# Kernel tuning notes

Measured on AMD Instinct MI355X. Metric: run time of the kernel, lower is better.

## Reference

```python
import jax, jax.numpy as jnp
import numpy as np

B, N, D = 8, 9856, 256
HEADS = 8
WH, WW = 7, 11
HID = 512  # int(D * 2.0)
EPS = 1e-5


def layernorm(x, g, b):
    mu = jnp.mean(x, axis=-1, keepdims=True)
    var = jnp.mean(jnp.square(x - mu), axis=-1, keepdims=True)
    return (x - mu) * jax.lax.rsqrt(var + EPS) * g + b


def setup_inputs() -> dict:
    key = jax.random.key(0)
    ks = jax.random.split(key, 6)
    s = lambda k, shape: (jax.random.normal(k, shape, jnp.float32) * 0.02)
    return {
        "x": jax.random.normal(ks[0], (B, N, D), jnp.float32),
        "norm1_g": jnp.ones((D,), jnp.float32),
        "norm1_b": jnp.zeros((D,), jnp.float32),
        "in_proj_w": s(ks[1], (3 * D, D)),
        "in_proj_b": jnp.zeros((3 * D,), jnp.float32),
        "out_w": s(ks[2], (D, D)),
        "out_b": jnp.zeros((D,), jnp.float32),
        "norm2_g": jnp.ones((D,), jnp.float32),
        "norm2_b": jnp.zeros((D,), jnp.float32),
        "fc1_w": s(ks[3], (HID, D)),
        "fc1_b": jnp.zeros((HID,), jnp.float32),
        "fc2_w": s(ks[4], (D, HID)),
        "fc2_b": jnp.zeros((D,), jnp.float32),
        "h": 56,
        "w": 176,
    }


def reference(x, norm1_g, norm1_b, in_proj_w, in_proj_b, out_w, out_b,
              norm2_g, norm2_b, fc1_w, fc1_b, fc2_w, fc2_b, h, w):
    Bx, Nx, Dx = x.shape
    n_h, n_w = h // WH, w // WW  # chosen dims divide evenly -> pad_h = pad_w = 0
    hd = Dx // HEADS
    L = WH * WW  # 77 tokens per window

    res = x
    xn = layernorm(x, norm1_g, norm1_b)

    # window partition: (B, h*w, D) -> (B*n_h*n_w, wh*ww, D)
    win = xn.reshape(Bx, n_h, WH, n_w, WW, Dx)
    win = win.transpose(0, 1, 3, 2, 4, 5).reshape(-1, L, Dx)

    # MultiheadAttention (batch_first) on each window independently
    qkv = win @ in_proj_w.T + in_proj_b          # (NW, L, 3D)
    q, k, v = jnp.split(qkv, 3, axis=-1)
    NW = win.shape[0]
    q = q.reshape(NW, L, HEADS, hd).transpose(0, 2, 1, 3)
    k = k.reshape(NW, L, HEADS, hd).transpose(0, 2, 1, 3)
    v = v.reshape(NW, L, HEADS, hd).transpose(0, 2, 1, 3)
    scores = jnp.einsum("nhld,nhmd->nhlm", q, k) / jnp.sqrt(jnp.float32(hd))
    attn = jax.nn.softmax(scores, axis=-1)
    o = jnp.einsum("nhlm,nhmd->nhld", attn, v)   # (NW, H, L, hd)
    o = o.transpose(0, 2, 1, 3).reshape(NW, L, Dx)
    o = o @ out_w.T + out_b

    # window reverse: (B*n_h*n_w, wh*ww, D) -> (B, h*w, D)
    o = o.reshape(Bx, n_h, n_w, WH, WW, Dx)
    o = o.transpose(0, 1, 3, 2, 4, 5).reshape(Bx, Nx, Dx)

    x = res + o
    res = x
    xn2 = layernorm(x, norm2_g, norm2_b)
    hmid = jax.nn.gelu(xn2 @ fc1_w.T + fc1_b, approximate=False)
    mlp = hmid @ fc2_w.T + fc2_b
    return res + mlp
```

## Files before the change

kernel.cpp:

```cpp
#include <hip/hip_runtime.h>
#include <hip/hip_bf16.h>

typedef unsigned short u16;
typedef unsigned int   u32;

typedef __bf16 bf16x8 __attribute__((ext_vector_type(8)));
typedef float  f32x4  __attribute__((ext_vector_type(4)));

__device__ __forceinline__ u16 f2bf(float f) {
  u32 u = __float_as_uint(f);
  u += 0x7fffu + ((u >> 16) & 1u);
  return (u16)(u >> 16);
}
__device__ __forceinline__ u32 pack2(float a, float b) {
  return (u32)f2bf(a) | ((u32)f2bf(b) << 16);
}
__device__ __forceinline__ void gld16(const void* g, void* l) {
  __builtin_amdgcn_global_load_lds(
      (const __attribute__((address_space(1))) unsigned int*)g,
      (__attribute__((address_space(3))) unsigned int*)l, 16, 0, 0);
}

#define TOK_M   78848
#define DIM     256
#define NWIN    1024
#define WINL    77

__global__ __launch_bounds__(256)
void cvt_w(const float* __restrict__ w0, const float* __restrict__ w1,
           const float* __restrict__ w2, const float* __restrict__ w3,
           u16* __restrict__ out)
{
  const int i = (blockIdx.x * 256 + threadIdx.x) * 4;
  const float* src; int off;
  if      (i < 196608) { src = w0; off = i; }
  else if (i < 262144) { src = w1; off = i - 196608; }
  else if (i < 393216) { src = w2; off = i - 262144; }
  else                 { src = w3; off = i - 393216; }
  float4 v = *(const float4*)(src + off);
  uint2 o; o.x = pack2(v.x, v.y); o.y = pack2(v.z, v.w);
  *(uint2*)(out + i) = o;
}

template<bool PERM>
__global__ __launch_bounds__(256)
void ln_k(const float* __restrict__ X, const float* __restrict__ g,
          const float* __restrict__ bta, u16* __restrict__ Y)
{
  const int tid  = threadIdx.x;
  const int tok  = blockIdx.x * 4 + (tid >> 6);
  const int lane = tid & 63;
  float4 v = *(const float4*)(X + (size_t)tok * DIM + lane * 4);
  float s = v.x + v.y + v.z + v.w;
#pragma unroll
  for (int off = 32; off; off >>= 1) s += __shfl_xor(s, off);
  const float mu = s * (1.f / 256.f);
  const float dx = v.x - mu, dy = v.y - mu, dz = v.z - mu, dw = v.w - mu;
  float q = dx * dx + dy * dy + dz * dz + dw * dw;
#pragma unroll
  for (int off = 32; off; off >>= 1) q += __shfl_xor(q, off);
  const float rstd = rsqrtf(q * (1.f / 256.f) + 1e-5f);
  float4 gg = *(const float4*)(g + lane * 4);
  float4 bb = *(const float4*)(bta + lane * 4);
  const float y0 = dx * rstd * gg.x + bb.x;
  const float y1 = dy * rstd * gg.y + bb.y;
  const float y2 = dz * rstd * gg.z + bb.z;
  const float y3 = dw * rstd * gg.w + bb.w;
  size_t dest = (size_t)tok;
  if (PERM) {
    const int b  = tok / 9856, n = tok - b * 9856;
    const int y  = n / 176,  xc = n - y * 176;
    const int ih = y / 7,    rr = y - ih * 7;
    const int iw = xc / 11,  cc = xc - iw * 11;
    dest = (size_t)(((b * 8 + ih) * 16 + iw)) * 77 + rr * 11 + cc;
  }
  uint2 o;
  o.x = pack2(y0, y1);
  o.y = pack2(y2, y3);
  *(uint2*)(Y + dest * DIM + lane * 4) = o;
}

template<int EPI, int OBF>
__global__ __launch_bounds__(256, 3)
void gemm_mfma(const u16* __restrict__ A, const u16* __restrict__ W,
               const float* __restrict__ bias, const float* res,
               void* Cout, int N, int K)
{
  __shared__ u16 As[4096];
  __shared__ u16 Bs[4096];

  const int tid  = threadIdx.x;
  const int wave = tid >> 6, lane = tid & 63;
  const int wy = wave >> 1, wx = wave & 1;
  const int quad = lane >> 4, l16 = lane & 15;
  const int m0 = blockIdx.x * 128;
  const int n0 = blockIdx.y * 128;

  const int s0 = tid, s1 = tid + 256;
  const int r0 = s0 >> 2, r1 = s1 >> 2;
  const int kb0 = (s0 & 3) ^ (r0 & 3);
  const int kb1 = (s1 & 3) ^ (r1 & 3);
  const u16* Ag0 = A + (size_t)(m0 + r0) * K + kb0 * 8;
  const u16* Ag1 = A + (size_t)(m0 + r1) * K + kb1 * 8;
  const u16* Bg0 = W + (size_t)(n0 + r0) * K + kb0 * 8;
  const u16* Bg1 = W + (size_t)(n0 + r1) * K + kb1 * 8;

  const int kbs = quad ^ (l16 & 3);
  const u16* Ar = &As[(wy * 64 + l16) * 32 + kbs * 8];
  const u16* Br = &Bs[(wx * 64 + l16) * 32 + kbs * 8];

  f32x4 acc[4][4];
#pragma unroll
  for (int i = 0; i < 4; ++i)
#pragma unroll
    for (int j = 0; j < 4; ++j) {
      f32x4 z = {0.f, 0.f, 0.f, 0.f};
      acc[i][j] = z;
    }

  for (int kt = 0; kt < K; kt += 32) {
    gld16(Ag0 + kt, &As[s0 * 8]);
    gld16(Ag1 + kt, &As[s1 * 8]);
    gld16(Bg0 + kt, &Bs[s0 * 8]);
    gld16(Bg1 + kt, &Bs[s1 * 8]);
    __syncthreads();
    bf16x8 af[4], bv[4];
#pragma unroll
    for (int i = 0; i < 4; ++i) {
      af[i] = *(const bf16x8*)(Ar + i * 16 * 32);
      bv[i] = *(const bf16x8*)(Br + i * 16 * 32);
    }
#pragma unroll
    for (int mi = 0; mi < 4; ++mi)
#pragma unroll
      for (int ni = 0; ni < 4; ++ni)
        acc[mi][ni] = __builtin_amdgcn_mfma_f32_16x16x32_bf16(
            af[mi], bv[ni], acc[mi][ni], 0, 0, 0);
    __syncthreads();
  }

  const int gr0 = m0 + wy * 64 + quad * 4;
  const int gc0 = n0 + wx * 64 + l16;
#pragma unroll
  for (int ni = 0; ni < 4; ++ni) {
    const int gc = gc0 + ni * 16;
    const float bvs = bias[gc];
#pragma unroll
    for (int mi = 0; mi < 4; ++mi) {
      const int gr = gr0 + mi * 16;
      f32x4 a = acc[mi][ni];
#pragma unroll
      for (int e = 0; e < 4; ++e) {
        float v = a[e] + bvs;
        const size_t idx = (size_t)(gr + e) * N + gc;
        if (EPI == 1) v += res[idx];
        else if (EPI == 2) v = 0.5f * v * (1.f + erff(v * 0.70710678118654752f));
        if (OBF) ((u16*)Cout)[idx] = f2bf(v);
        else     ((float*)Cout)[idx] = v;
      }
    }
  }
}

#define PSTR 104
__global__ __launch_bounds__(128)
void attn_mfma(const u16* __restrict__ qkv, u16* __restrict__ onat)
{
  __shared__ __bf16 Pb[2][80 * PSTR];

  const int tid  = threadIdx.x;
  const int wave = tid >> 6, lane = tid & 63;
  const int quad = lane >> 4, l16 = lane & 15;
  const int pair = blockIdx.x * 2 + wave;
  const int nw   = pair >> 3, head = pair & 7;
  const size_t base = (size_t)nw * 77 * 768;
  const int hoff = head * 32;
  __bf16* P = Pb[wave];

  {
    uint4 z = {0, 0, 0, 0};
    for (int r = lane; r < 80; r += 64) {
      *(uint4*)(P + r * PSTR + 80) = z;
      *(uint4*)(P + r * PSTR + 88) = z;
    }
  }

  bf16x8 qf[5], kf[5];
  const u16* qp = qkv + base + hoff + quad * 8;
#pragma unroll
  for (int mi = 0; mi < 5; ++mi) {
    const size_t row = (size_t)(l16 + 16 * mi) * 768;
    qf[mi] = *(const bf16x8*)(qp + row);
    kf[mi] = *(const bf16x8*)(qp + row + 256);
  }

  f32x4 s[5][5];
#pragma unroll
  for (int mi = 0; mi < 5; ++mi)
#pragma unroll
    for (int ni = 0; ni < 5; ++ni) {
      f32x4 z = {0.f, 0.f, 0.f, 0.f};
      s[mi][ni] = z;
    }
#pragma unroll
  for (int mi = 0; mi < 5; ++mi)
#pragma unroll
    for (int ni = 0; ni < 5; ++ni)
      s[mi][ni] = __builtin_amdgcn_mfma_f32_16x16x32_bf16(
          qf[mi], kf[ni], s[mi][ni], 0, 0, 0);

  bf16x8 vf[3][2];
  {
    const __bf16* vbb = (const __bf16*)(qkv + base + 512 + hoff + l16);
#pragma unroll
    for (int ks = 0; ks < 3; ++ks)
#pragma unroll
      for (int ni = 0; ni < 2; ++ni)
#pragma unroll
        for (int jj = 0; jj < 8; ++jj) {
          const int k = ks * 32 + quad * 8 + jj;
          vf[ks][ni][jj] = (k < 77) ? vbb[(size_t)k * 768 + 16 * ni] : (__bf16)0.f;
        }
  }

  if (l16 >= 13) {
#pragma unroll
    for (int mi = 0; mi < 5; ++mi)
#pragma unroll
      for (int e = 0; e < 4; ++e) s[mi][4][e] = -1e30f;
  }

  const float c = 0.17677669529663687f * 1.4426950408889634f;
  float inv[5][4];
#pragma unroll
  for (int mi = 0; mi < 5; ++mi)
#pragma unroll
    for (int e = 0; e < 4; ++e) {
      float mx = s[mi][0][e];
#pragma unroll
      for (int ni = 1; ni < 5; ++ni) mx = fmaxf(mx, s[mi][ni][e]);
#pragma unroll
      for (int off = 1; off < 16; off <<= 1) mx = fmaxf(mx, __shfl_xor(mx, off));
      float sum = 0.f;
#pragma unroll
      for (int ni = 0; ni < 5; ++ni) {
        const float ev = exp2f((s[mi][ni][e] - mx) * c);
        s[mi][ni][e] = ev;
        sum += ev;
      }
#pragma unroll
      for (int off = 1; off < 16; off <<= 1) sum += __shfl_xor(sum, off);
      inv[mi][e] = 1.f / sum;
    }

#pragma unroll
  for (int mi = 0; mi < 5; ++mi)
#pragma unroll
    for (int e = 0; e < 4; ++e) {
      const int m = quad * 4 + e + 16 * mi;
#pragma unroll
      for (int ni = 0; ni < 5; ++ni)
        P[m * PSTR + l16 + 16 * ni] = (__bf16)(s[mi][ni][e] * inv[mi][e]);
    }

  f32x4 o[5][2];
#pragma unroll
  for (int mi = 0; mi < 5; ++mi)
#pragma unroll
    for (int ni = 0; ni < 2; ++ni) {
      f32x4 z = {0.f, 0.f, 0.f, 0.f};
      o[mi][ni] = z;
    }
#pragma unroll
  for (int ks = 0; ks < 3; ++ks)
#pragma unroll
    for (int mi = 0; mi < 5; ++mi) {
      const bf16x8 af = *(const bf16x8*)(P + (l16 + 16 * mi) * PSTR + ks * 32 + quad * 8);
#pragma unroll
      for (int ni = 0; ni < 2; ++ni)
        o[mi][ni] = __builtin_amdgcn_mfma_f32_16x16x32_bf16(
            af, vf[ks][ni], o[mi][ni], 0, 0, 0);
    }

  const int b  = nw >> 7;
  const int ih = (nw >> 4) & 7;
  const int iw = nw & 15;
#pragma unroll
  for (int mi = 0; mi < 5; ++mi)
#pragma unroll
    for (int e = 0; e < 4; ++e) {
      const int t = quad * 4 + e + 16 * mi;
      if (t < 77) {
        const int rr = t / 11, cc = t - rr * 11;
        const int y = ih * 7 + rr, xc = iw * 11 + cc;
        const size_t nat = (size_t)b * 9856 + (size_t)y * 176 + xc;
        u16* dst = onat + nat * DIM + hoff + l16;
        dst[0]  = f2bf(o[mi][0][e]);
        dst[16] = f2bf(o[mi][1][e]);
      }
    }
}

extern "C" void kernel_launch(void* const* d_in, const int* in_sizes, int n_in,
                              void* d_out, int out_size, void* d_ws, size_t ws_size,
                              hipStream_t stream)
{
  (void)in_sizes; (void)n_in; (void)out_size; (void)ws_size;
  const float* x    = (const float*)d_in[0];
  const float* g1   = (const float*)d_in[1];
  const float* b1   = (const float*)d_in[2];
  const float* wqkv = (const float*)d_in[3];
  const float* bqkv = (const float*)d_in[4];
  const float* wout = (const float*)d_in[5];
  const float* bout = (const float*)d_in[6];
  const float* g2   = (const float*)d_in[7];
  const float* b2   = (const float*)d_in[8];
  const float* w1   = (const float*)d_in[9];
  const float* bf1  = (const float*)d_in[10];
  const float* w2   = (const float*)d_in[11];
  const float* bf2  = (const float*)d_in[12];

  char* ws = (char*)d_ws;
  u16*   qkv  = (u16*)(ws);
  u16*   xn   = (u16*)(ws + 121110528);
  u16*   onat = (u16*)(ws + 161480704);
  u16*   wb   = (u16*)(ws + 201850880);
  u16*   wqkv_b = wb;
  u16*   wout_b = wb + 196608;
  u16*   w1_b   = wb + 262144;
  u16*   w2_b   = wb + 393216;
  float* x2   = (float*)d_out;

  cvt_w<<<512, 256, 0, stream>>>(wqkv, wout, w1, w2, wb);
  ln_k<true><<<19712, 256, 0, stream>>>(x, g1, b1, xn);
  gemm_mfma<0, 1><<<dim3(616, 6), 256, 0, stream>>>(xn, wqkv_b, bqkv, nullptr, qkv, 768, 256);
  attn_mfma<<<4096, 128, 0, stream>>>(qkv, onat);
  gemm_mfma<1, 0><<<dim3(616, 2), 256, 0, stream>>>(onat, wout_b, bout, x, x2, 256, 256);
  ln_k<false><<<19712, 256, 0, stream>>>(x2, g2, b2, xn);
  gemm_mfma<2, 1><<<dim3(616, 4), 256, 0, stream>>>(xn, w1_b, bf1, nullptr, qkv, 512, 256);
  gemm_mfma<1, 0><<<dim3(616, 2), 256, 0, stream>>>(qkv, w2_b, bf2, x2, x2, 256, 512);
}
```

Measured before the change: 597.3 us.

## Double-buffer GEMM LDS tiles and swap grid order for A-tile reuse

The MFMA GEMM now uses two LDS buffers per operand and issues the global-to-LDS loads for the next K tile before computing on the current one, so load latency overlaps with MFMA work. The grid is also transposed so that consecutive blocks share the same A row tile across N tiles, which should improve L2 reuse of the activation matrix. LDS use per block doubles, which may reduce occupancy below the launch-bounds target. The visible loop keeps a single barrier, so whether the buffer being overwritten is safely separated from reads of the previous iteration depends on the unseen end of the loop.

```diff
diff --git a/kernel.cpp b/kernel.cpp
--- a/kernel.cpp
+++ b/kernel.cpp
@@ -86,15 +86,15 @@
                const float* __restrict__ bias, const float* res,
                void* Cout, int N, int K)
 {
-  __shared__ u16 As[4096];
-  __shared__ u16 Bs[4096];
+  __shared__ u16 As[2][4096];
+  __shared__ u16 Bs[2][4096];
 
   const int tid  = threadIdx.x;
   const int wave = tid >> 6, lane = tid & 63;
   const int wy = wave >> 1, wx = wave & 1;
   const int quad = lane >> 4, l16 = lane & 15;
-  const int m0 = blockIdx.x * 128;
-  const int n0 = blockIdx.y * 128;
+  const int m0 = blockIdx.y * 128;
+  const int n0 = blockIdx.x * 128;
 
   const int s0 = tid, s1 = tid + 256;
   const int r0 = s0 >> 2, r1 = s1 >> 2;
@@ -106,8 +106,8 @@
   const u16* Bg1 = W + (size_t)(n0 + r1) * K + kb1 * 8;
 
   const int kbs = quad ^ (l16 & 3);
-  const u16* Ar = &As[(wy * 64 + l16) * 32 + kbs * 8];
-  const u16* Br = &Bs[(wx * 64 + l16) * 32 + kbs * 8];
+  const int aoff = (wy * 64 + l16) * 32 + kbs * 8;
+  const int boff = (wx * 64 + l16) * 32 + kbs * 8;
 
   f32x4 acc[4][4];
 #pragma unroll
@@ -118,12 +118,24 @@
       acc[i][j] = z;
     }
 
-  for (int kt = 0; kt < K; kt += 32) {
-    gld16(Ag0 + kt, &As[s0 * 8]);
-    gld16(Ag1 + kt, &As[s1 * 8]);
-    gld16(Bg0 + kt, &Bs[s0 * 8]);
-    gld16(Bg1 + kt, &Bs[s1 * 8]);
-    __syncthreads();
+  gld16(Ag0, &As[0][s0 * 8]);
+  gld16(Ag1, &As[0][s1 * 8]);
+  gld16(Bg0, &Bs[0][s0 * 8]);
+  gld16(Bg1, &Bs[0][s1 * 8]);
+  __syncthreads();
+
+  const int NT = K >> 5;
+  for (int t = 0; t < NT; ++t) {
+    const int cur = t & 1;
+    if (t + 1 < NT) {
+      const int kt = (t + 1) << 5;
+      gld16(Ag0 + kt, &As[cur ^ 1][s0 * 8]);
+      gld16(Ag1 + kt, &As[cur ^ 1][s1 * 8]);
+      gld16(Bg0 + kt, &Bs[cur ^ 1][s0 * 8]);
+      gld16(Bg1 + kt, &Bs[cur ^ 1][s1 * 8]);
+    }
+    const u16* Ar = &As[cur][aoff];
+    const u16* Br = &Bs[cur][boff];
     bf16x8 af[4], bv[4];
 #pragma unroll
     for (int i = 0; i < 4; ++i) {
@@ -333,10 +345,10 @@
 
   cvt_w<<<512, 256, 0, stream>>>(wqkv, wout, w1, w2, wb);
   ln_k<true><<<19712, 256, 0, stream>>>(x, g1, b1, xn);
-  gemm_mfma<0, 1><<<dim3(616, 6), 256, 0, stream>>>(xn, wqkv_b, bqkv, nullptr, qkv, 768, 256);
+  gemm_mfma<0, 1><<<dim3(6, 616), 256, 0, stream>>>(xn, wqkv_b, bqkv, nullptr, qkv, 768, 256);
   attn_mfma<<<4096, 128, 0, stream>>>(qkv, onat);
-  gemm_mfma<1, 0><<<dim3(616, 2), 256, 0, stream>>>(onat, wout_b, bout, x, x2, 256, 256);
+  gemm_mfma<1, 0><<<dim3(2, 616), 256, 0, stream>>>(onat, wout_b, bout, x, x2, 256, 256);
   ln_k<false><<<19712, 256, 0, stream>>>(x2, g2, b2, xn);
-  gemm_mfma<2, 1><<<dim3(616, 4), 256, 0, stream>>>(xn, w1_b, bf1, nullptr, qkv, 512, 256);
-  gemm_mfma<1, 0><<<dim3(616, 2), 256, 0, stream>>>(qkv, w2_b, bf2, x2, x2, 256, 512);
-}
+  gemm_mfma<2, 1><<<dim3(4, 616), 256, 0, stream>>>(xn, w1_b, bf1, nullptr, qkv, 512, 256);
+  gemm_mfma<1, 0><<<dim3(2, 616), 256, 0, stream>>>(qkv, w2_b, bf2, x2, x2, 256, 512);
+}
```

Measured after the change: 582.6 us. 1.03x faster.

## Keep weight panels resident in LDS and stream A rows persistently

Applied to the files above, without the earlier changes.

Weights are now converted into an MFMA-fragment-ordered panel layout so each GEMM block loads its whole weight panel (128 columns × K) into LDS once. The block then loops persistently over row tiles, reading A fragments straight from global memory into registers. This removes the per-k-step LDS staging of A and B and the two barriers per iteration, and avoids reloading weights for every row tile. The cost is a 64KB LDS footprint that limits occupancy, plus A loads that go uncached through LDS with possibly poor coalescing.

```diff
diff --git a/kernel.cpp b/kernel.cpp
--- a/kernel.cpp
+++ b/kernel.cpp
@@ -26,20 +26,37 @@
 #define NWIN    1024
 #define WINL    77
 
+template<int K, int NF>
+__device__ __forceinline__ void cvt_chunk(const float* __restrict__ src,
+                                          u16* __restrict__ dst, int rel)
+{
+  constexpr int KT = K / 32;
+  constexpr int PN = NF * 16;
+  const int lane  = rel & 63;
+  const int g     = rel >> 6;
+  const int nf    = g % NF;
+  const int kt    = (g / NF) % KT;
+  const int panel = g / (NF * KT);
+  const int col   = panel * PN + nf * 16 + (lane & 15);
+  const int k0    = kt * 32 + (lane >> 4) * 8;
+  const float4 a = *(const float4*)(src + (size_t)col * K + k0);
+  const float4 b = *(const float4*)(src + (size_t)col * K + k0 + 4);
+  uint4 o;
+  o.x = pack2(a.x, a.y); o.y = pack2(a.z, a.w);
+  o.z = pack2(b.x, b.y); o.w = pack2(b.z, b.w);
+  *(uint4*)(dst + (size_t)rel * 8) = o;
+}
+
 __global__ __launch_bounds__(256)
 void cvt_w(const float* __restrict__ w0, const float* __restrict__ w1,
            const float* __restrict__ w2, const float* __restrict__ w3,
            u16* __restrict__ out)
 {
-  const int i = (blockIdx.x * 256 + threadIdx.x) * 4;
-  const float* src; int off;
-  if      (i < 196608) { src = w0; off = i; }
-  else if (i < 262144) { src = w1; off = i - 196608; }
-  else if (i < 393216) { src = w2; off = i - 262144; }
-  else                 { src = w3; off = i - 393216; }
-  float4 v = *(const float4*)(src + off);
-  uint2 o; o.x = pack2(v.x, v.y); o.y = pack2(v.z, v.w);
-  *(uint2*)(out + i) = o;
+  const int c = blockIdx.x * 256 + threadIdx.x;
+  if      (c < 24576) cvt_chunk<256, 8>(w0, out,          c);
+  else if (c < 32768) cvt_chunk<256, 8>(w1, out + 196608, c - 24576);
+  else if (c < 49152) cvt_chunk<256, 8>(w2, out + 262144, c - 32768);
+  else                cvt_chunk<512, 4>(w3, out + 393216, c - 49152);
 }
 
 template<bool PERM>
@@ -80,83 +97,72 @@
   *(uint2*)(Y + dest * DIM + lane * 4) = o;
 }
 
-template<int EPI, int OBF>
-__global__ __launch_bounds__(256, 3)
-void gemm_mfma(const u16* __restrict__ A, const u16* __restrict__ W,
-               const float* __restrict__ bias, const float* res,
-               void* Cout, int N, int K)
-{
-  __shared__ u16 As[4096];
-  __shared__ u16 Bs[4096];
+template<int K, int NF, int EPI, int OBF>
+__global__ __launch_bounds__(256, 2)
+void gemm2(const u16* __restrict__ A, const u16* __restrict__ W2,
+           const float* __restrict__ bias, const float* __restrict__ res,
+           void* __restrict__ Cout, int N)
+{
+  constexpr int KT = K / 32;
+  constexpr int PN = NF * 16;
+  __shared__ u16 Bp[PN * K];
 
   const int tid  = threadIdx.x;
   const int wave = tid >> 6, lane = tid & 63;
-  const int wy = wave >> 1, wx = wave & 1;
   const int quad = lane >> 4, l16 = lane & 15;
-  const int m0 = blockIdx.x * 128;
-  const int n0 = blockIdx.y * 128;
-
-  const int s0 = tid, s1 = tid + 256;
-  const int r0 = s0 >> 2, r1 = s1 >> 2;
-  const int kb0 = (s0 & 3) ^ (r0 & 3);
-  const int kb1 = (s1 & 3) ^ (r1 & 3);
-  const u16* Ag0 = A + (size_t)(m0 + r0) * K + kb0 * 8;
-  const u16* Ag1 = A + (size_t)(m0 + r1) * K + kb1 * 8;
-  const u16* Bg0 = W + (size_t)(n0 + r0) * K + kb0 * 8;
-  const u16* Bg1 = W + (size_t)(n0 + r1) * K + kb1 * 8;
-
-  const int kbs = quad ^ (l16 & 3);
-  const u16* Ar = &As[(wy * 64 + l16) * 32 + kbs * 8];
-  const u16* Br = &Bs[(wx * 64 + l16) * 32 + kbs * 8];
-
-  f32x4 acc[4][4];
-#pragma unroll
-  for (int i = 0; i < 4; ++i)
-#pragma unroll
-    for (int j = 0; j < 4; ++j) {
-      f32x4 z = {0.f, 0.f, 0.f, 0.f};
-      acc[i][j] = z;
-    }
-
-  for (int kt = 0; kt < K; kt += 32) {
-    gld16(Ag0 + kt, &As[s0 * 8]);
-    gld16(Ag1 + kt, &As[s1 * 8]);
-    gld16(Bg0 + kt, &Bs[s0 * 8]);
-    gld16(Bg1 + kt, &Bs[s1 * 8]);
-    __syncthreads();
-    bf16x8 af[4], bv[4];
-#pragma unroll
-    for (int i = 0; i < 4; ++i) {
-      af[i] = *(const bf16x8*)(Ar + i * 16 * 32);
-      bv[i] = *(const bf16x8*)(Br + i * 16 * 32);
-    }
-#pragma unroll
-    for (int mi = 0; mi < 4; ++mi)
-#pragma unroll
-      for (int ni = 0; ni < 4; ++ni)
-        acc[mi][ni] = __builtin_amdgcn_mfma_f32_16x16x32_bf16(
-            af[mi], bv[ni], acc[mi][ni], 0, 0, 0);
-    __syncthreads();
-  }
-
-  const int gr0 = m0 + wy * 64 + quad * 4;
-  const int gc0 = n0 + wx * 64 + l16;
-#pragma unroll
-  for (int ni = 0; ni < 4; ++ni) {
-    const int gc = gc0 + ni * 16;
-    const float bvs = bias[gc];
-#pragma unroll
-    for (int mi = 0; mi < 4; ++mi) {
-      const int gr = gr0 + mi * 16;
-      f32x4 a = acc[mi][ni];
-#pragma unroll
-      for (int e = 0; e < 4; ++e) {
-        float v = a[e] + bvs;
-        const size_t idx = (size_t)(gr + e) * N + gc;
-        if (EPI == 1) v += res[idx];
-        else if (EPI == 2) v = 0.5f * v * (1.f + erff(v * 0.70710678118654752f));
-        if (OBF) ((u16*)Cout)[idx] = f2bf(v);
-        else     ((float*)Cout)[idx] = v;
+
+  {
+    const u16* src = W2 + (size_t)blockIdx.x * (PN * K) + tid * 8;
+    u16* dst = Bp + tid * 8;
+#pragma unroll
+    for (int i = 0; i < (PN * K) / 2048; ++i)
+      gld16(src + i * 2048, dst + i * 2048);
+  }
+  __syncthreads();
+
+  const int n0 = blockIdx.x * PN;
+  for (int s = blockIdx.y; s < 616; s += gridDim.y) {
+    const int row0 = s * 128 + wave * 32;
+    const u16* A0 = A + (size_t)(row0 + l16) * K + quad * 8;
+
+    f32x4 acc[2][NF];
+#pragma unroll
+    for (int mi = 0; mi < 2; ++mi)
+#pragma unroll
+      for (int nf = 0; nf < NF; ++nf) {
+        f32x4 z = {0.f, 0.f, 0.f, 0.f};
+        acc[mi][nf] = z;
+      }
+
+#pragma unroll
+    for (int kt = 0; kt < KT; ++kt) {
+      const bf16x8 af0 = *(const bf16x8*)(A0 + kt * 32);
+      const bf16x8 af1 = *(const bf16x8*)(A0 + (size_t)16 * K + kt * 32);
+#pragma unroll
+      for (int nf = 0; nf < NF; ++nf) {
+        const bf16x8 bf = *(const bf16x8*)(Bp + (kt * NF + nf) * 512 + lane * 8);
+        acc[0][nf] = __builtin_amdgcn_mfma_f32_16x16x32_bf16(af0, bf, acc[0][nf], 0, 0, 0);
+        acc[1][nf] = __builtin_amdgcn_mfma_f32_16x16x32_bf16(af1, bf, acc[1][nf], 0, 0, 0);
+      }
+    }
+
+#pragma unroll
+    for (int nf = 0; nf < NF; ++nf) {
+      const int col = n0 + nf * 16 + l16;
+      const float bvs = bias[col];
+#pragma unroll
+      for (int mi = 0; mi < 2; ++mi) {
+        const int r0 = row0 + mi * 16 + quad * 4;
+        f32x4 a = acc[mi][nf];
+#pragma unroll
+        for (int e = 0; e < 4; ++e) {
+          float v = a[e] + bvs;
+          const size_t idx = (size_t)(r0 + e) * N + col;
+          if (EPI == 1) v += res[idx];
+          else if (EPI == 2) v = 0.5f * v * (1.f + erff(v * 0.70710678118654752f));
+          if (OBF) ((u16*)Cout)[idx] = f2bf(v);
+          else     ((float*)Cout)[idx] = v;
+        }
       }
     }
   }
@@ -331,12 +337,12 @@
   u16*   w2_b   = wb + 393216;
   float* x2   = (float*)d_out;
 
-  cvt_w<<<512, 256, 0, stream>>>(wqkv, wout, w1, w2, wb);
+  cvt_w<<<256, 256, 0, stream>>>(wqkv, wout, w1, w2, wb);
   ln_k<true><<<19712, 256, 0, stream>>>(x, g1, b1, xn);
-  gemm_mfma<0, 1><<<dim3(616, 6), 256, 0, stream>>>(xn, wqkv_b, bqkv, nullptr, qkv, 768, 256);
+  gemm2<256, 8, 0, 1><<<dim3(6, 85),  256, 0, stream>>>(xn,   wqkv_b, bqkv, nullptr, qkv, 768);
   attn_mfma<<<4096, 128, 0, stream>>>(qkv, onat);
-  gemm_mfma<1, 0><<<dim3(616, 2), 256, 0, stream>>>(onat, wout_b, bout, x, x2, 256, 256);
+  gemm2<256, 8, 1, 0><<<dim3(2, 256), 256, 0, stream>>>(onat, wout_b, bout, x,  x2, 256);
   ln_k<false><<<19712, 256, 0, stream>>>(x2, g2, b2, xn);
-  gemm_mfma<2, 1><<<dim3(616, 4), 256, 0, stream>>>(xn, w1_b, bf1, nullptr, qkv, 512, 256);
-  gemm_mfma<1, 0><<<dim3(616, 2), 256, 0, stream>>>(qkv, w2_b, bf2, x2, x2, 256, 512);
-}
+  gemm2<256, 8, 2, 1><<<dim3(4, 128), 256, 0, stream>>>(xn,   w1_b,   bf1,  nullptr, qkv, 512);
+  gemm2<512, 4, 1, 0><<<dim3(4, 128), 256, 0, stream>>>(qkv,  w2_b,   bf2,  x2, x2, 256);
+}
```

Result: slower. 821.6 us (+37.5%).
